# Kernel optimization log

Measured on AMD Instinct MI355X. Metric: run time of the kernel, lower is better.

## Reference

```python
import jax, jax.numpy as jnp
import numpy as np

EPS_AGG = 1e-6
EPS_BN = 1e-5
EPS_LN = 1e-5


def _bn(t, g, b):
    # BatchNorm1d in training mode: batch statistics over dim 0
    m = t.mean(0)
    v = t.var(0)
    return (t - m) * jax.lax.rsqrt(v + EPS_BN) * g + b


def _gated_gcn(x, e, src, dst, Aw, Ab, Bw, Bb, Cw, Cb, Dw, Db, Ew, Eb, gx, bx, ge, be):
    # GraphGPS GatedGCNLayer (residual=True, dropout=0, no PE)
    N = x.shape[0]
    Ax = x @ Aw + Ab
    Bx = x @ Bw + Bb
    Ce = e @ Cw + Cb
    Dx = x @ Dw + Db
    Ex = x @ Ew + Eb
    e_new = Dx[dst] + Ex[src] + Ce            # [E, D] edge gates (i=target, j=source)
    sig = jax.nn.sigmoid(e_new)
    num = jax.ops.segment_sum(sig * Bx[src], dst, num_segments=N)
    den = jax.ops.segment_sum(sig, dst, num_segments=N) + EPS_AGG
    x_new = Ax + num / den
    x = x + jax.nn.relu(_bn(x_new, gx, bx))   # BN -> ReLU -> residual
    e = e + jax.nn.relu(_bn(e_new, ge, be))
    return x, e


def setup_inputs() -> dict:
    key = jax.random.key(0)
    G, NPG, DEG, D = 256, 32, 8, 70
    NC, H = 10, 256
    N, E = G * NPG, G * NPG * DEG
    ks = list(jax.random.split(key, 24))

    def nrm(k, shape):
        return jax.random.normal(k, shape, jnp.float32)

    def lin(k, i, o):
        return nrm(k, (i, o)) / np.float32(np.sqrt(i)), jnp.zeros((o,), jnp.float32)

    x = nrm(ks[0], (N, 1))
    edge_attr = nrm(ks[1], (E, 1))
    base = jnp.repeat(jnp.arange(G, dtype=jnp.int32) * NPG, NPG * DEG)
    src = base + jax.random.randint(ks[2], (E,), 0, NPG, dtype=jnp.int32)
    dst = base + jax.random.randint(ks[3], (E,), 0, NPG, dtype=jnp.int32)
    edge_index = jnp.stack([src, dst])
    batch_index = jnp.repeat(jnp.arange(G, dtype=jnp.int32), NPG)

    inp = {"x": x, "edge_index": edge_index, "edge_attr": edge_attr, "batch_index": batch_index}
    inp["w_node"], inp["b_node"] = lin(ks[4], 1, D)
    inp["w_edge"], inp["b_edge"] = lin(ks[5], 1, D)
    i = 6
    for l in ("1", "2"):
        for nm in ("A", "B", "C", "D", "E"):
            inp[nm + l + "w"], inp[nm + l + "b"] = lin(ks[i], D, D)
            i += 1
        inp["gx" + l], inp["bx" + l] = jnp.ones((D,), jnp.float32), jnp.zeros((D,), jnp.float32)
        inp["ge" + l], inp["be" + l] = jnp.ones((D,), jnp.float32), jnp.zeros((D,), jnp.float32)
    inp["cls1_w"], inp["cls1_b"] = lin(ks[i], 2 * D, H)
    i += 1
    inp["ln_g"], inp["ln_b"] = jnp.ones((H,), jnp.float32), jnp.zeros((H,), jnp.float32)
    inp["cls2_w"], inp["cls2_b"] = lin(ks[i], H, NC)
    return inp


def reference(x, edge_index, edge_attr, batch_index,
              w_node, b_node, w_edge, b_edge,
              A1w, A1b, B1w, B1b, C1w, C1b, D1w, D1b, E1w, E1b, gx1, bx1, ge1, be1,
              A2w, A2b, B2w, B2b, C2w, C2b, D2w, D2b, E2w, E2b, gx2, bx2, ge2, be2,
              cls1_w, cls1_b, ln_g, ln_b, cls2_w, cls2_b):
    src, dst = edge_index[0], edge_index[1]
    bi = np.asarray(batch_index)
    n_iters = int(np.bincount(bi).max() // 2)   # int(max(sizes)/2)
    B = int(bi.max()) + 1

    h = x @ w_node + b_node
    e = edge_attr @ w_edge + b_edge
    h, e = _gated_gcn(h, e, src, dst, A1w, A1b, B1w, B1b, C1w, C1b, D1w, D1b, E1w, E1b, gx1, bx1, ge1, be1)
    for _ in range(n_iters):  # shared conv2 weights
        h, e = _gated_gcn(h, e, src, dst, A2w, A2b, B2w, B2b, C2w, C2b, D2w, D2b, E2w, E2b, gx2, bx2, ge2, be2)

    gmp = jax.ops.segment_max(h, batch_index, num_segments=B)
    cnt = jax.ops.segment_sum(jnp.ones((h.shape[0], 1), h.dtype), batch_index, num_segments=B)
    gap = jax.ops.segment_sum(h, batch_index, num_segments=B) / cnt
    g = jnp.concatenate([gmp, gap], axis=1)            # [B, 2*D]
    g = jax.nn.relu(g @ cls1_w + cls1_b)               # [B, 256]
    mu = g.mean(-1, keepdims=True)
    var = g.var(-1, keepdims=True)
    g = (g - mu) * jax.lax.rsqrt(var + EPS_LN) * ln_g + ln_b
    return g @ cls2_w + cls2_b                         # [B, num_classes]
```

## Files before the change

### kernel.cpp

```cpp
#include <hip/hip_runtime.h>
#include <hip/hip_fp16.h>
#include <math.h>


#define TPB 768
#define NBLK 256
#define DD 70
#define ETS 256
#define NBS 84
#define SLS 80
#define NLAYERS 17
#define SPL 280
#define NSLOT 8
#define EPS_AGG 1e-6f
#define EPS_BN 1e-5f
#define EPS_LN 1e-5f

#define SCX 0
#define SHX 72
#define SCE 144
#define SHE 216
#define SBO 288
#define BAO 360
#define BBO 432
#define ZBO 504
#define STATL_F 576

#define OFF_ET   0
#define OFF_HN   (OFF_ET + 72*ETS)
#define OFF_AX   (OFF_HN + 32*NBS)
#define OFF_BX   (OFF_AX + 32*NBS)
#define OFF_DX   (OFF_BX + 32*NBS)
#define OFF_EX   (OFF_DX + 32*NBS)
#define OFF_SLAB (OFF_EX + 32*NBS)
#define OFF_STATL (OFF_SLAB + 72*SLS)
#define SMEM_FLOATS (OFF_STATL + STATL_F)
#define SMEM_BYTES  (SMEM_FLOATS*4 + (32+33)*4 + 512 + 512 + 16)

#define EIX(k,e) (((k)<<8) + ((e) ^ ((((k)>>2)&7)<<2)))
#define SIX(j,c) (((j)<<7) + ((c) ^ ((j)&30)))

struct GPSParams {
  const float* __restrict__ x; const int* __restrict__ ei; const float* __restrict__ ea;
  const float* __restrict__ wn; const float* __restrict__ bnn;
  const float* __restrict__ we; const float* __restrict__ web;
  const float* __restrict__ Aw[2]; const float* __restrict__ Ab[2];
  const float* __restrict__ Bw[2]; const float* __restrict__ Bb[2];
  const float* __restrict__ Cw[2]; const float* __restrict__ Cb[2];
  const float* __restrict__ Dw[2]; const float* __restrict__ Db[2];
  const float* __restrict__ Ew[2]; const float* __restrict__ Eb[2];
  const float* __restrict__ gx[2]; const float* __restrict__ bx[2];
  const float* __restrict__ ge[2]; const float* __restrict__ gbe[2];
  const float* __restrict__ c1w; const float* __restrict__ c1b;
  const float* __restrict__ lng; const float* __restrict__ lnb;
  const float* __restrict__ c2w; const float* __restrict__ c2b;
  float* __restrict__ out; float* __restrict__ stats; unsigned* __restrict__ bar;
};

__device__ __forceinline__ void grid_sync(unsigned* b) {
  __syncthreads();
  if (threadIdx.x == 0) {
    unsigned g = __hip_atomic_load(b, __ATOMIC_RELAXED, __HIP_MEMORY_SCOPE_AGENT);
    int leaf = (int)(blockIdx.x >> 4);
    unsigned a = __hip_atomic_fetch_add(b + 32 + leaf*32, 1u, __ATOMIC_ACQ_REL, __HIP_MEMORY_SCOPE_AGENT);
    bool done = false;
    if (a == 15u) {
      unsigned r = __hip_atomic_fetch_add(b + 16, 1u, __ATOMIC_ACQ_REL, __HIP_MEMORY_SCOPE_AGENT);
      if (r == 15u) {
        #pragma unroll
        for (int i2 = 0; i2 < 16; ++i2)
          __hip_atomic_store(b + 32 + i2*32, 0u, __ATOMIC_RELAXED, __HIP_MEMORY_SCOPE_AGENT);
        __hip_atomic_store(b + 16, 0u, __ATOMIC_RELAXED, __HIP_MEMORY_SCOPE_AGENT);
        __hip_atomic_store(b, g + 1u, __ATOMIC_RELEASE, __HIP_MEMORY_SCOPE_AGENT);
        done = true;
      }
    }
    if (!done) {
      while (__hip_atomic_load(b, __ATOMIC_ACQUIRE, __HIP_MEMORY_SCOPE_AGENT) == g)
        __builtin_amdgcn_s_sleep(2);
    }
  }
  __syncthreads();
}

__device__ __forceinline__ void stage_wt(float* __restrict__ slab,
                                         const float* __restrict__ W, int tid) {
  for (int i = tid; i < 72*SLS; i += TPB) {
    int j = i / SLS, K = i % SLS;
    slab[i] = (j < DD && K < DD) ? W[K*DD + j] : 0.f;
  }
}

__global__ void __launch_bounds__(TPB)
__attribute__((amdgpu_waves_per_eu(3, 3)))
gps_kernel(GPSParams p) {
  extern __shared__ float smem[];
  float* eT    = smem + OFF_ET;
  float* hN    = smem + OFF_HN;
  float* Ax    = smem + OFF_AX;
  float* Bx    = smem + OFF_BX;
  float* Dx    = smem + OFF_DX;
  float* Ex    = smem + OFF_EX;
  float* slab  = smem + OFF_SLAB;
  float* statl = smem + OFF_STATL;
  unsigned* sigb = (unsigned*)(smem + OFF_DX);
  const __half* sigh = (const __half*)sigb;
  int*   icur  = (int*)(smem + SMEM_FLOATS);
  int*   ioff  = icur + 32;
  unsigned char* srcloc = (unsigned char*)(ioff + 33);
  unsigned char* dstloc = srcloc + 256;
  unsigned short* eidxS = (unsigned short*)(dstloc + 256);

  const int tid  = threadIdx.x;
  const int g    = blockIdx.x;
  const int lane = tid & 63;
  const int wid  = tid >> 6;

  const int jbe = wid * 6;
  const int e0  = lane * 4;
  const int n_kh = lane >> 5;
  const int n_n  = lane & 31;
  const int n_k0 = n_kh * 40;

  float* slot = p.stats + ((g & 7) * NLAYERS) * SPL;

  if (tid < 32) icur[tid] = 0;
  __syncthreads();
  if (tid < 256) {
    int s0 = p.ei[g*256 + tid]         - g*32;
    int d0 = p.ei[65536 + g*256 + tid] - g*32;
    srcloc[tid] = (unsigned char)s0;
    dstloc[tid] = (unsigned char)d0;
    atomicAdd(&icur[d0], 1);
  }
  __syncthreads();
  if (tid == 0) {
    int o = 0;
    for (int n = 0; n < 32; ++n) { ioff[n] = o; o += icur[n]; }
    ioff[32] = o;
  }
  __syncthreads();
  if (tid < 32) icur[tid] = ioff[tid];
  __syncthreads();
  if (tid < 256) {
    int d0 = dstloc[tid];
    int sl2 = atomicAdd(&icur[d0], 1);
    eidxS[sl2] = (unsigned short)(tid | ((int)srcloc[tid] << 8));
  }

  for (int i = tid; i < 5*32*NBS; i += TPB) hN[i] = 0.f;
  for (int i = tid; i < STATL_F; i += TPB) statl[i] = 0.f;
  for (int i = tid; i < 2*ETS; i += TPB) eT[70*ETS + i] = 0.f;
  __syncthreads();
  for (int i = tid; i < 32*DD; i += TPB) {
    int n = i / DD, j = i % DD;
    hN[n*NBS + j] = fmaf(p.x[g*32 + n], p.wn[j], p.bnn[j]);
  }
  for (int i = tid; i < DD*256; i += TPB) {
    int k = i >> 8, e = i & 255;
    eT[EIX(k, e)] = fmaf(p.ea[g*256 + e], p.we[k], p.web[k]);
  }
  __syncthreads();

  auto node_phase = [&](const float* __restrict__ W, float* __restrict__ nbuf, int boff) {
    stage_wt(slab, W, tid);
    __syncthreads();
    float acc[6];
    #pragma unroll
    for (int i = 0; i < 6; ++i) acc[i] = 0.f;
    const float* hrow = hN + n_n*NBS + n_k0;
    #pragma unroll
    for (int c = 0; c < 5; ++c) {
      float4 ha = *(const float4*)(hrow + c*8);
      float4 hb = *(const float4*)(hrow + c*8 + 4);
      #pragma unroll
      for (int i = 0; i < 6; ++i) {
        const float* wr = slab + (jbe + i)*SLS + n_k0 + c*8;
        float4 wa = *(const float4*)(wr);
        float4 wb = *(const float4*)(wr + 4);
        acc[i] = fmaf(ha.x, wa.x, acc[i]); acc[i] = fmaf(ha.y, wa.y, acc[i]);
        acc[i] = fmaf(ha.z, wa.z, acc[i]); acc[i] = fmaf(ha.w, wa.w, acc[i]);
        acc[i] = fmaf(hb.x, wb.x, acc[i]); acc[i] = fmaf(hb.y, wb.y, acc[i]);
        acc[i] = fmaf(hb.z, wb.z, acc[i]); acc[i] = fmaf(hb.w, wb.w, acc[i]);
      }
    }
    #pragma unroll
    for (int i = 0; i < 6; ++i) acc[i] += __shfl_xor(acc[i], 32, 64);
    if (n_kh == 0) {
      #pragma unroll
      for (int i = 0; i < 6; ++i) {
        int j = jbe + i;
        if (j < DD) nbuf[n_n*NBS + j] = acc[i] + statl[boff + j];
      }
    }
    __syncthreads();
  };

  #pragma unroll 1
  for (int L = 0; L < NLAYERS; ++L) {
    const int s = (L == 0) ? 0 : 1;
    float* lslot = slot + L * SPL;

    if (tid < DD) {
      statl[BAO + tid] = p.Ab[s][tid];
      statl[BBO + tid] = p.Bb[s][tid];
      statl[SBO + tid] = p.Cb[s][tid] + p.Db[s][tid] + p.Eb[s][tid];
    }
    node_phase(p.Aw[s], Ax, BAO);
    node_phase(p.Bw[s], Bx, BBO);
    node_phase(p.Dw[s], Dx, ZBO);
    node_phase(p.Ew[s], Ex, ZBO);

    stage_wt(slab, p.Cw[s], tid);
    __syncthreads();

    float acc[4][6];
    #pragma unroll
    for (int r = 0; r < 4; ++r)
      #pragma unroll
      for (int i = 0; i < 6; ++i) acc[r][i] = 0.f;

    #pragma unroll 2
    for (int c = 0; c < 18; ++c) {
      const int k0 = c*4;
      float4 ev0 = *(const float4*)(eT + EIX(k0+0, e0));
      float4 ev1 = *(const float4*)(eT + EIX(k0+1, e0));
      float4 ev2 = *(const float4*)(eT + EIX(k0+2, e0));
      float4 ev3 = *(const float4*)(eT + EIX(k0+3, e0));
      #pragma unroll
      for (int i = 0; i < 6; ++i) {
        float4 w4 = *(const float4*)(slab + (jbe + i)*SLS + k0);
        acc[0][i] = fmaf(ev0.x, w4.x, acc[0][i]); acc[1][i] = fmaf(ev0.y, w4.x, acc[1][i]);
        acc[2][i] = fmaf(ev0.z, w4.x, acc[2][i]); acc[3][i] = fmaf(ev0.w, w4.x, acc[3][i]);
        acc[0][i] = fmaf(ev1.x, w4.y, acc[0][i]); acc[1][i] = fmaf(ev1.y, w4.y, acc[1][i]);
        acc[2][i] = fmaf(ev1.z, w4.y, acc[2][i]); acc[3][i] = fmaf(ev1.w, w4.y, acc[3][i]);
        acc[0][i] = fmaf(ev2.x, w4.z, acc[0][i]); acc[1][i] = fmaf(ev2.y, w4.z, acc[1][i]);
        acc[2][i] = fmaf(ev2.z, w4.z, acc[2][i]); acc[3][i] = fmaf(ev2.w, w4.z, acc[3][i]);
        acc[0][i] = fmaf(ev3.x, w4.w, acc[0][i]); acc[1][i] = fmaf(ev3.y, w4.w, acc[1][i]);
        acc[2][i] = fmaf(ev3.z, w4.w, acc[2][i]); acc[3][i] = fmaf(ev3.w, w4.w, acc[3][i]);
      }
    }

    {
      int dl0 = dstloc[e0],   sl0 = srcloc[e0];
      int dl1 = dstloc[e0+1], sl1 = srcloc[e0+1];
      int dl2 = dstloc[e0+2], sl2 = srcloc[e0+2];
      int dl3 = dstloc[e0+3], sl3 = srcloc[e0+3];
      #pragma unroll
      for (int i = 0; i < 6; ++i) {
        int j = jbe + i;
        if (j < DD) {
          float bb = statl[SBO + j];
          acc[0][i] += Dx[dl0*NBS + j] + Ex[sl0*NBS + j] + bb;
          acc[1][i] += Dx[dl1*NBS + j] + Ex[sl1*NBS + j] + bb;
          acc[2][i] += Dx[dl2*NBS + j] + Ex[sl2*NBS + j] + bb;
          acc[3][i] += Dx[dl3*NBS + j] + Ex[sl3*NBS + j] + bb;
        }
      }
    }

    #pragma unroll
    for (int i = 0; i < 6; ++i) {
      int j = jbe + i;
      float ps = (acc[0][i] + acc[1][i]) + (acc[2][i] + acc[3][i]);
      float qs = acc[0][i]*acc[0][i];
      qs = fmaf(acc[1][i], acc[1][i], qs);
      qs = fmaf(acc[2][i], acc[2][i], qs);
      qs = fmaf(acc[3][i], acc[3][i], qs);
      #pragma unroll
      for (int d = 1; d < 64; d <<= 1) {
        ps += __shfl_xor(ps, d, 64);
        qs += __shfl_xor(qs, d, 64);
      }
      if (lane == 0 && j < DD) {
        atomicAdd(lslot + 140 + j, ps);
        atomicAdd(lslot + 210 + j, qs);
      }
    }
    __syncthreads();

    #pragma unroll
    for (int i = 0; i < 6; ++i) {
      int j = jbe + i;
      if (j < DD) {
        float s0 = 1.f / (1.f + __expf(-acc[0][i]));
        float s1 = 1.f / (1.f + __expf(-acc[1][i]));
        float s2 = 1.f / (1.f + __expf(-acc[2][i]));
        float s3 = 1.f / (1.f + __expf(-acc[3][i]));
        __half2 h01 = __floats2half2_rn(s0, s1);
        __half2 h23 = __floats2half2_rn(s2, s3);
        uint2 pk;
        pk.x = *reinterpret_cast<unsigned*>(&h01);
        pk.y = *reinterpret_cast<unsigned*>(&h23);
        *reinterpret_cast<uint2*>(sigb + SIX(j, 2*lane)) = pk;
      }
    }
    __syncthreads();

    if (tid < 576) {
      int n = tid / 18, jq = tid % 18;
      int j0 = jq * 4;
      bool v2 = (j0 + 2) < DD, v3 = (j0 + 3) < DD;
      float nm0 = 0.f, nm1 = 0.f, nm2 = 0.f, nm3 = 0.f;
      float dn0 = 0.f, dn1 = 0.f, dn2 = 0.f, dn3 = 0.f;
      int pb = ioff[n], pe = ioff[n + 1];
      for (int pp = pb; pp < pe; ++pp) {
        unsigned v = eidxS[pp];
        int e2 = v & 255, sl2 = v >> 8;
        int cb = e2 >> 1, h2 = e2 & 1;
        float s0 = __half2float(sigh[(SIX(j0+0, cb) << 1) + h2]);
        float s1 = __half2float(sigh[(SIX(j0+1, cb) << 1) + h2]);
        float s2 = v2 ? __half2float(sigh[(SIX(j0+2, cb) << 1) + h2]) : 0.f;
        float s3 = v3 ? __half2float(sigh[(SIX(j0+3, cb) << 1) + h2]) : 0.f;
        float4 b4 = *(const float4*)(Bx + sl2*NBS + j0);
        nm0 = fmaf(s0, b4.x, nm0); nm1 = fmaf(s1, b4.y, nm1);
        nm2 = fmaf(s2, b4.z, nm2); nm3 = fmaf(s3, b4.w, nm3);
        dn0 += s0; dn1 += s1; dn2 += s2; dn3 += s3;
      }
      float* axp = Ax + n*NBS + j0;
      float4 ax = *(const float4*)axp;
      ax.x += nm0 / (dn0 + EPS_AGG);
      ax.y += nm1 / (dn1 + EPS_AGG);
      ax.z += nm2 / (dn2 + EPS_AGG);
      ax.w += nm3 / (dn3 + EPS_AGG);
      *(float4*)axp = ax;
    }
    __syncthreads();

    if (tid < SPL) {
      int col = tid % DD, q = tid / DD;
      float sm = 0.f, sq = 0.f;
      #pragma unroll
      for (int r = 0; r < 8; ++r) {
        float v = Ax[(q*8 + r)*NBS + col];
        sm += v; sq = fmaf(v, v, sq);
      }
      atomicAdd(lslot + col, sm);
      atomicAdd(lslot + 70 + col, sq);
    }

    grid_sync(p.bar);

    if (tid < DD) {
      float sm = 0.f, sq = 0.f;
      #pragma unroll
      for (int sl2 = 0; sl2 < NSLOT; ++sl2) {
        const float* st = p.stats + (sl2*NLAYERS + L)*SPL;
        sm += __hip_atomic_load(st + tid,      __ATOMIC_RELAXED, __HIP_MEMORY_SCOPE_AGENT);
        sq += __hip_atomic_load(st + 70 + tid, __ATOMIC_RELAXED, __HIP_MEMORY_SCOPE_AGENT);
      }
      float mean = sm * (1.f/8192.f);
      float var  = sq * (1.f/8192.f) - mean*mean;
      float sc = p.gx[s][tid] * rsqrtf(var + EPS_BN);
      statl[SCX + tid] = sc;
      statl[SHX + tid] = fmaf(-mean, sc, p.bx[s][tid]);
    } else if (tid < 140) {
      int j = tid - DD;
      float sm = 0.f, sq = 0.f;
      #pragma unroll
      for (int sl2 = 0; sl2 < NSLOT; ++sl2) {
        const float* st = p.stats + (sl2*NLAYERS + L)*SPL;
        sm += __hip_atomic_load(st + 140 + j, __ATOMIC_RELAXED, __HIP_MEMORY_SCOPE_AGENT);
        sq += __hip_atomic_load(st + 210 + j, __ATOMIC_RELAXED, __HIP_MEMORY_SCOPE_AGENT);
      }
      float mean = sm * (1.f/65536.f);
      float var  = sq * (1.f/65536.f) - mean*mean;
      float sc = p.ge[s][j] * rsqrtf(var + EPS_BN);
      statl[SCE + j] = sc;
      statl[SHE + j] = fmaf(-mean, sc, p.gbe[s][j]);
    }
    __syncthreads();

    #pragma unroll
    for (int r = 0; r < 3; ++r) {
      int idx = tid + r*TPB;
      int n = idx / 72, j = idx - n*72;
      if (j < DD) {
        float xn = Ax[n*NBS + j];
        hN[n*NBS + j] += fmaxf(fmaf(xn, statl[SCX + j], statl[SHX + j]), 0.f);
      }
    }
    #pragma unroll
    for (int i = 0; i < 6; ++i) {
      int j = jbe + i;
      if (j < DD) {
        float sc = statl[SCE + j], sh = statl[SHE + j];
        float* ep = eT + EIX(j, e0);
        float4 eo = *(const float4*)ep;
        eo.x += fmaxf(fmaf(acc[0][i], sc, sh), 0.f);
        eo.y += fmaxf(fmaf(acc[1][i], sc, sh), 0.f);
        eo.z += fmaxf(fmaf(acc[2][i], sc, sh), 0.f);
        eo.w += fmaxf(fmaf(acc[3][i], sc, sh), 0.f);
        *(float4*)ep = eo;
      }
    }
    __syncthreads();
  }

  if (tid < DD) {
    float mx = -3.4e38f, sm = 0.f;
    #pragma unroll 4
    for (int r = 0; r < 32; ++r) {
      float v = hN[r*NBS + tid];
      mx = fmaxf(mx, v); sm += v;
    }
    statl[tid]      = mx;
    statl[70 + tid] = sm * (1.f/32.f);
  }
  __syncthreads();
  if (tid < 256) {
    float a = p.c1b[tid];
    for (int k = 0; k < DD; ++k) a = fmaf(statl[k],      p.c1w[k*256 + tid], a);
    for (int k = 0; k < DD; ++k) a = fmaf(statl[70 + k], p.c1w[(DD + k)*256 + tid], a);
    Ax[tid] = fmaxf(a, 0.f);
  }
  __syncthreads();
  if (tid == 0) {
    float sm = 0.f, sq = 0.f;
    for (int k = 0; k < 256; ++k) { float v = Ax[k]; sm += v; sq = fmaf(v, v, sq); }
    float mean = sm * (1.f/256.f);
    float var  = sq * (1.f/256.f) - mean*mean;
    statl[560] = mean;
    statl[561] = rsqrtf(var + EPS_LN);
  }
  __syncthreads();
  if (tid < 256) {
    float v = (Ax[tid] - statl[560]) * statl[561];
    Bx[tid] = fmaf(v, p.lng[tid], p.lnb[tid]);
  }
  __syncthreads();
  if (tid < 10) {
    float a = p.c2b[tid];
    for (int k = 0; k < 256; ++k) a = fmaf(Bx[k], p.c2w[k*10 + tid], a);
    p.out[g*10 + tid] = a;
  }
}

extern "C" void kernel_launch(void* const* d_in, const int* in_sizes, int n_in,
                              void* d_out, int out_size, void* d_ws, size_t ws_size,
                              hipStream_t stream) {
  (void)in_sizes; (void)n_in; (void)out_size; (void)ws_size;
  GPSParams p;
  p.x   = (const float*)d_in[0];
  p.ei  = (const int*)  d_in[1];
  p.ea  = (const float*)d_in[2];
  p.wn  = (const float*)d_in[4];  p.bnn = (const float*)d_in[5];
  p.we  = (const float*)d_in[6];  p.web = (const float*)d_in[7];
  int i = 8;
  for (int s = 0; s < 2; ++s) {
    p.Aw[s] = (const float*)d_in[i++]; p.Ab[s] = (const float*)d_in[i++];
    p.Bw[s] = (const float*)d_in[i++]; p.Bb[s] = (const float*)d_in[i++];
    p.Cw[s] = (const float*)d_in[i++]; p.Cb[s] = (const float*)d_in[i++];
    p.Dw[s] = (const float*)d_in[i++]; p.Db[s] = (const float*)d_in[i++];
    p.Ew[s] = (const float*)d_in[i++]; p.Eb[s] = (const float*)d_in[i++];
    p.gx[s] = (const float*)d_in[i++]; p.bx[s] = (const float*)d_in[i++];
    p.ge[s] = (const float*)d_in[i++]; p.gbe[s] = (const float*)d_in[i++];
  }
  p.c1w = (const float*)d_in[36]; p.c1b = (const float*)d_in[37];
  p.lng = (const float*)d_in[38]; p.lnb = (const float*)d_in[39];
  p.c2w = (const float*)d_in[40]; p.c2b = (const float*)d_in[41];
  p.out = (float*)d_out;
  p.bar = (unsigned*)d_ws;
  p.stats = (float*)((char*)d_ws + 4096);

  hipMemsetAsync(d_ws, 0, 4096 + NSLOT*NLAYERS*SPL*4, stream);

  hipFuncSetAttribute((const void*)gps_kernel,
                      hipFuncAttributeMaxDynamicSharedMemorySize, SMEM_BYTES);

  void* args[] = { (void*)&p };
  hipError_t err = hipLaunchCooperativeKernel((const void*)gps_kernel,
                                              dim3(NBLK), dim3(TPB),
                                              args, SMEM_BYTES, stream);
  if (err != hipSuccess) {
    gps_kernel<<<dim3(NBLK), dim3(TPB), SMEM_BYTES, stream>>>(p);
  }
}
```

Baseline: 1.063 ms.

## Pre-transpose weights into global workspace once and fuse four node GEMMs into one pass

Ten blocks transpose and pad all A/B/C/D/E weight matrices into a global workspace once, then a grid sync publishes them. Every block now reads weights directly from global/L2 instead of restaging each matrix into LDS five times per layer. The four separate node-projection phases, each with its own barriers, are merged into one phase where wave groups compute A, B, D and E concurrently with a 3x4 register tile. This removes many per-layer LDS staging passes and __syncthreads, at the cost of one extra grid-wide barrier and uncached-in-LDS global weight loads inside the inner loops.

Result: no change. 1.068 ms (+0.5%).

```diff
diff --git a/kernel.cpp b/kernel.cpp
--- a/kernel.cpp
+++ b/kernel.cpp
@@ -8,7 +8,7 @@
 #define DD 70
 #define ETS 256
 #define NBS 84
-#define SLS 80
+#define WTS 80
 #define NLAYERS 17
 #define SPL 280
 #define NSLOT 8
@@ -21,9 +21,6 @@
 #define SCE 144
 #define SHE 216
 #define SBO 288
-#define BAO 360
-#define BBO 432
-#define ZBO 504
 #define STATL_F 576
 
 #define OFF_ET   0
@@ -32,13 +29,16 @@
 #define OFF_BX   (OFF_AX + 32*NBS)
 #define OFF_DX   (OFF_BX + 32*NBS)
 #define OFF_EX   (OFF_DX + 32*NBS)
-#define OFF_SLAB (OFF_EX + 32*NBS)
-#define OFF_STATL (OFF_SLAB + 72*SLS)
+#define OFF_PAD  (OFF_EX + 32*NBS)
+#define OFF_STATL (OFF_PAD + 3584)
 #define SMEM_FLOATS (OFF_STATL + STATL_F)
 #define SMEM_BYTES  (SMEM_FLOATS*4 + (32+33)*4 + 512 + 512 + 16)
 
 #define EIX(k,e) (((k)<<8) + ((e) ^ ((((k)>>2)&7)<<2)))
 #define SIX(j,c) (((j)<<7) + ((c) ^ ((j)&30)))
+
+#define WS_STATS 4096
+#define WS_WT    163840
 
 struct GPSParams {
   const float* __restrict__ x; const int* __restrict__ ei; const float* __restrict__ ea;
@@ -54,7 +54,8 @@
   const float* __restrict__ c1w; const float* __restrict__ c1b;
   const float* __restrict__ lng; const float* __restrict__ lnb;
   const float* __restrict__ c2w; const float* __restrict__ c2b;
-  float* __restrict__ out; float* __restrict__ stats; unsigned* __restrict__ bar;
+  float* __restrict__ out; float* __restrict__ stats; float* __restrict__ wt;
+  unsigned* __restrict__ bar;
 };
 
 __device__ __forceinline__ void grid_sync(unsigned* b) {
@@ -83,14 +84,6 @@
   __syncthreads();
 }
 
-__device__ __forceinline__ void stage_wt(float* __restrict__ slab,
-                                         const float* __restrict__ W, int tid) {
-  for (int i = tid; i < 72*SLS; i += TPB) {
-    int j = i / SLS, K = i % SLS;
-    slab[i] = (j < DD && K < DD) ? W[K*DD + j] : 0.f;
-  }
-}
-
 __global__ void __launch_bounds__(TPB)
 __attribute__((amdgpu_waves_per_eu(3, 3)))
 gps_kernel(GPSParams p) {
@@ -101,7 +94,6 @@
   float* Bx    = smem + OFF_BX;
   float* Dx    = smem + OFF_DX;
   float* Ex    = smem + OFF_EX;
-  float* slab  = smem + OFF_SLAB;
   float* statl = smem + OFF_STATL;
   unsigned* sigb = (unsigned*)(smem + OFF_DX);
   const __half* sigh = (const __half*)sigb;
@@ -118,9 +110,9 @@
 
   const int jbe = wid * 6;
   const int e0  = lane * 4;
-  const int n_kh = lane >> 5;
-  const int n_n  = lane & 31;
-  const int n_k0 = n_kh * 40;
+  const int n_m  = wid & 3;
+  const int n_jb = (wid >> 2) * 24 + (lane >> 3) * 3;
+  const int n_n0 = (lane & 7) * 4;
 
   float* slot = p.stats + ((g & 7) * NLAYERS) * SPL;
 
@@ -148,8 +140,7 @@
     eidxS[sl2] = (unsigned short)(tid | ((int)srcloc[tid] << 8));
   }
 
-  for (int i = tid; i < 5*32*NBS; i += TPB) hN[i] = 0.f;
-  for (int i = tid; i < STATL_F; i += TPB) statl[i] = 0.f;
+  for (int i = tid; i < SMEM_FLOATS - OFF_HN; i += TPB) smem[OFF_HN + i] = 0.f;
   for (int i = tid; i < 2*ETS; i += TPB) eT[70*ETS + i] = 0.f;
   __syncthreads();
   for (int i = tid; i < 32*DD; i += TPB) {
@@ -160,65 +151,76 @@
     int k = i >> 8, e = i & 255;
     eT[EIX(k, e)] = fmaf(p.ea[g*256 + e], p.we[k], p.web[k]);
   }
-  __syncthreads();
-
-  auto node_phase = [&](const float* __restrict__ W, float* __restrict__ nbuf, int boff) {
-    stage_wt(slab, W, tid);
-    __syncthreads();
-    float acc[6];
-    #pragma unroll
-    for (int i = 0; i < 6; ++i) acc[i] = 0.f;
-    const float* hrow = hN + n_n*NBS + n_k0;
-    #pragma unroll
-    for (int c = 0; c < 5; ++c) {
-      float4 ha = *(const float4*)(hrow + c*8);
-      float4 hb = *(const float4*)(hrow + c*8 + 4);
-      #pragma unroll
-      for (int i = 0; i < 6; ++i) {
-        const float* wr = slab + (jbe + i)*SLS + n_k0 + c*8;
-        float4 wa = *(const float4*)(wr);
-        float4 wb = *(const float4*)(wr + 4);
-        acc[i] = fmaf(ha.x, wa.x, acc[i]); acc[i] = fmaf(ha.y, wa.y, acc[i]);
-        acc[i] = fmaf(ha.z, wa.z, acc[i]); acc[i] = fmaf(ha.w, wa.w, acc[i]);
-        acc[i] = fmaf(hb.x, wb.x, acc[i]); acc[i] = fmaf(hb.y, wb.y, acc[i]);
-        acc[i] = fmaf(hb.z, wb.z, acc[i]); acc[i] = fmaf(hb.w, wb.w, acc[i]);
-      }
-    }
-    #pragma unroll
-    for (int i = 0; i < 6; ++i) acc[i] += __shfl_xor(acc[i], 32, 64);
-    if (n_kh == 0) {
-      #pragma unroll
-      for (int i = 0; i < 6; ++i) {
-        int j = jbe + i;
-        if (j < DD) nbuf[n_n*NBS + j] = acc[i] + statl[boff + j];
-      }
-    }
-    __syncthreads();
-  };
+
+  if (g < 10) {
+    int ss = g / 5, mm = g % 5;
+    const float* W = (mm==0) ? p.Aw[ss] : (mm==1) ? p.Bw[ss] : (mm==2) ? p.Cw[ss]
+                   : (mm==3) ? p.Dw[ss] : p.Ew[ss];
+    float* dst = p.wt + g * (72*WTS);
+    for (int i = tid; i < 72*WTS; i += TPB) {
+      int j = i / WTS, k = i - j*WTS;
+      dst[i] = (j < DD && k < DD) ? W[k*DD + j] : 0.f;
+    }
+  }
+  grid_sync(p.bar);
 
   #pragma unroll 1
   for (int L = 0; L < NLAYERS; ++L) {
     const int s = (L == 0) ? 0 : 1;
     float* lslot = slot + L * SPL;
-
-    if (tid < DD) {
-      statl[BAO + tid] = p.Ab[s][tid];
-      statl[BBO + tid] = p.Bb[s][tid];
-      statl[SBO + tid] = p.Cb[s][tid] + p.Db[s][tid] + p.Eb[s][tid];
-    }
-    node_phase(p.Aw[s], Ax, BAO);
-    node_phase(p.Bw[s], Bx, BBO);
-    node_phase(p.Dw[s], Dx, ZBO);
-    node_phase(p.Ew[s], Ex, ZBO);
-
-    stage_wt(slab, p.Cw[s], tid);
-    __syncthreads();
-
-    float acc[4][6];
+    const float* wbase = p.wt + (size_t)(s*5) * (72*WTS);
+
+    if (tid < DD) statl[SBO + tid] = p.Cb[s][tid] + p.Db[s][tid] + p.Eb[s][tid];
+
+    {
+      const float* Wm = wbase + ((n_m==0) ? 0 : (n_m==1) ? 1 : (n_m==2) ? 3 : 4) * (72*WTS);
+      float* nbuf = (n_m==0) ? Ax : (n_m==1) ? Bx : (n_m==2) ? Dx : Ex;
+      const float* nbias = (n_m==1) ? p.Bb[s] : p.Ab[s];
+      float acc[3][4];
+      #pragma unroll
+      for (int i = 0; i < 3; ++i)
+        #pragma unroll
+        for (int n = 0; n < 4; ++n) acc[i][n] = 0.f;
+      const float* hr0 = hN + n_n0*NBS;
+      #pragma unroll 2
+      for (int c = 0; c < 18; ++c) {
+        const int k0 = c*4;
+        float4 h0 = *(const float4*)(hr0 + 0*NBS + k0);
+        float4 h1 = *(const float4*)(hr0 + 1*NBS + k0);
+        float4 h2 = *(const float4*)(hr0 + 2*NBS + k0);
+        float4 h3 = *(const float4*)(hr0 + 3*NBS + k0);
+        #pragma unroll
+        for (int i = 0; i < 3; ++i) {
+          float4 w4 = *(const float4*)(Wm + (n_jb + i)*WTS + k0);
+          acc[i][0] = fmaf(h0.x, w4.x, acc[i][0]); acc[i][0] = fmaf(h0.y, w4.y, acc[i][0]);
+          acc[i][0] = fmaf(h0.z, w4.z, acc[i][0]); acc[i][0] = fmaf(h0.w, w4.w, acc[i][0]);
+          acc[i][1] = fmaf(h1.x, w4.x, acc[i][1]); acc[i][1] = fmaf(h1.y, w4.y, acc[i][1]);
+          acc[i][1] = fmaf(h1.z, w4.z, acc[i][1]); acc[i][1] = fmaf(h1.w, w4.w, acc[i][1]);
+          acc[i][2] = fmaf(h2.x, w4.x, acc[i][2]); acc[i][2] = fmaf(h2.y, w4.y, acc[i][2]);
+          acc[i][2] = fmaf(h2.z, w4.z, acc[i][2]); acc[i][2] = fmaf(h2.w, w4.w, acc[i][2]);
+          acc[i][3] = fmaf(h3.x, w4.x, acc[i][3]); acc[i][3] = fmaf(h3.y, w4.y, acc[i][3]);
+          acc[i][3] = fmaf(h3.z, w4.z, acc[i][3]); acc[i][3] = fmaf(h3.w, w4.w, acc[i][3]);
+        }
+      }
+      #pragma unroll
+      for (int i = 0; i < 3; ++i) {
+        int j = n_jb + i;
+        if (j < DD) {
+          float b = (n_m < 2) ? nbias[j] : 0.f;
+          #pragma unroll
+          for (int n = 0; n < 4; ++n)
+            nbuf[(n_n0 + n)*NBS + j] = acc[i][n] + b;
+        }
+      }
+    }
+    __syncthreads();
+
+    const float* wC = wbase + 2 * (72*WTS);
+    float eacc[4][6];
     #pragma unroll
     for (int r = 0; r < 4; ++r)
       #pragma unroll
-      for (int i = 0; i < 6; ++i) acc[r][i] = 0.f;
+      for (int i = 0; i < 6; ++i) eacc[r][i] = 0.f;
 
     #pragma unroll 2
     for (int c = 0; c < 18; ++c) {
@@ -229,15 +231,15 @@
       float4 ev3 = *(const float4*)(eT + EIX(k0+3, e0));
       #pragma unroll
       for (int i = 0; i < 6; ++i) {
-        float4 w4 = *(const float4*)(slab + (jbe + i)*SLS + k0);
-        acc[0][i] = fmaf(ev0.x, w4.x, acc[0][i]); acc[1][i] = fmaf(ev0.y, w4.x, acc[1][i]);
-        acc[2][i] = fmaf(ev0.z, w4.x, acc[2][i]); acc[3][i] = fmaf(ev0.w, w4.x, acc[3][i]);
-        acc[0][i] = fmaf(ev1.x, w4.y, acc[0][i]); acc[1][i] = fmaf(ev1.y, w4.y, acc[1][i]);
-        acc[2][i] = fmaf(ev1.z, w4.y, acc[2][i]); acc[3][i] = fmaf(ev1.w, w4.y, acc[3][i]);
-        acc[0][i] = fmaf(ev2.x, w4.z, acc[0][i]); acc[1][i] = fmaf(ev2.y, w4.z, acc[1][i]);
-        acc[2][i] = fmaf(ev2.z, w4.z, acc[2][i]); acc[3][i] = fmaf(ev2.w, w4.z, acc[3][i]);
-        acc[0][i] = fmaf(ev3.x, w4.w, acc[0][i]); acc[1][i] = fmaf(ev3.y, w4.w, acc[1][i]);
-        acc[2][i] = fmaf(ev3.z, w4.w, acc[2][i]); acc[3][i] = fmaf(ev3.w, w4.w, acc[3][i]);
+        float4 w4 = *(const float4*)(wC + (jbe + i)*WTS + k0);
+        eacc[0][i] = fmaf(ev0.x, w4.x, eacc[0][i]); eacc[1][i] = fmaf(ev0.y, w4.x, eacc[1][i]);
+        eacc[2][i] = fmaf(ev0.z, w4.x, eacc[2][i]); eacc[3][i] = fmaf(ev0.w, w4.x, eacc[3][i]);
+        eacc[0][i] = fmaf(ev1.x, w4.y, eacc[0][i]); eacc[1][i] = fmaf(ev1.y, w4.y, eacc[1][i]);
+        eacc[2][i] = fmaf(ev1.z, w4.y, eacc[2][i]); eacc[3][i] = fmaf(ev1.w, w4.y, eacc[3][i]);
+        eacc[0][i] = fmaf(ev2.x, w4.z, eacc[0][i]); eacc[1][i] = fmaf(ev2.y, w4.z, eacc[1][i]);
+        eacc[2][i] = fmaf(ev2.z, w4.z, eacc[2][i]); eacc[3][i] = fmaf(ev2.w, w4.z, eacc[3][i]);
+        eacc[0][i] = fmaf(ev3.x, w4.w, eacc[0][i]); eacc[1][i] = fmaf(ev3.y, w4.w, eacc[1][i]);
+        eacc[2][i] = fmaf(ev3.z, w4.w, eacc[2][i]); eacc[3][i] = fmaf(ev3.w, w4.w, eacc[3][i]);
       }
     }
 
@@ -251,10 +253,10 @@
         int j = jbe + i;
         if (j < DD) {
           float bb = statl[SBO + j];
-          acc[0][i] += Dx[dl0*NBS + j] + Ex[sl0*NBS + j] + bb;
-          acc[1][i] += Dx[dl1*NBS + j] + Ex[sl1*NBS + j] + bb;
-          acc[2][i] += Dx[dl2*NBS + j] + Ex[sl2*NBS + j] + bb;
-          acc[3][i] += Dx[dl3*NBS + j] + Ex[sl3*NBS + j] + bb;
+          eacc[0][i] += Dx[dl0*NBS + j] + Ex[sl0*NBS + j] + bb;
+          eacc[1][i] += Dx[dl1*NBS + j] + Ex[sl1*NBS + j] + bb;
+          eacc[2][i] += Dx[dl2*NBS + j] + Ex[sl2*NBS + j] + bb;
+          eacc[3][i] += Dx[dl3*NBS + j] + Ex[sl3*NBS + j] + bb;
         }
       }
     }
@@ -262,11 +264,11 @@
     #pragma unroll
     for (int i = 0; i < 6; ++i) {
       int j = jbe + i;
-      float ps = (acc[0][i] + acc[1][i]) + (acc[2][i] + acc[3][i]);
-      float qs = acc[0][i]*acc[0][i];
-      qs = fmaf(acc[1][i], acc[1][i], qs);
-      qs = fmaf(acc[2][i], acc[2][i], qs);
-      qs = fmaf(acc[3][i], acc[3][i], qs);
+      float ps = (eacc[0][i] + eacc[1][i]) + (eacc[2][i] + eacc[3][i]);
+      float qs = eacc[0][i]*eacc[0][i];
+      qs = fmaf(eacc[1][i], eacc[1][i], qs);
+      qs = fmaf(eacc[2][i], eacc[2][i], qs);
+      qs = fmaf(eacc[3][i], eacc[3][i], qs);
       #pragma unroll
       for (int d = 1; d < 64; d <<= 1) {
         ps += __shfl_xor(ps, d, 64);
@@ -283,10 +285,10 @@
     for (int i = 0; i < 6; ++i) {
       int j = jbe + i;
       if (j < DD) {
-        float s0 = 1.f / (1.f + __expf(-acc[0][i]));
-        float s1 = 1.f / (1.f + __expf(-acc[1][i]));
-        float s2 = 1.f / (1.f + __expf(-acc[2][i]));
-        float s3 = 1.f / (1.f + __expf(-acc[3][i]));
+        float s0 = 1.f / (1.f + __expf(-eacc[0][i]));
+        float s1 = 1.f / (1.f + __expf(-eacc[1][i]));
+        float s2 = 1.f / (1.f + __expf(-eacc[2][i]));
+        float s3 = 1.f / (1.f + __expf(-eacc[3][i]));
         __half2 h01 = __floats2half2_rn(s0, s1);
         __half2 h23 = __floats2half2_rn(s2, s3);
         uint2 pk;
@@ -387,10 +389,10 @@
         float sc = statl[SCE + j], sh = statl[SHE + j];
         float* ep = eT + EIX(j, e0);
         float4 eo = *(const float4*)ep;
-        eo.x += fmaxf(fmaf(acc[0][i], sc, sh), 0.f);
-        eo.y += fmaxf(fmaf(acc[1][i], sc, sh), 0.f);
-        eo.z += fmaxf(fmaf(acc[2][i], sc, sh), 0.f);
-        eo.w += fmaxf(fmaf(acc[3][i], sc, sh), 0.f);
+        eo.x += fmaxf(fmaf(eacc[0][i], sc, sh), 0.f);
+        eo.y += fmaxf(fmaf(eacc[1][i], sc, sh), 0.f);
+        eo.z += fmaxf(fmaf(eacc[2][i], sc, sh), 0.f);
+        eo.w += fmaxf(fmaf(eacc[3][i], sc, sh), 0.f);
         *(float4*)ep = eo;
       }
     }
@@ -461,9 +463,10 @@
   p.c2w = (const float*)d_in[40]; p.c2b = (const float*)d_in[41];
   p.out = (float*)d_out;
   p.bar = (unsigned*)d_ws;
-  p.stats = (float*)((char*)d_ws + 4096);
-
-  hipMemsetAsync(d_ws, 0, 4096 + NSLOT*NLAYERS*SPL*4, stream);
+  p.stats = (float*)((char*)d_ws + WS_STATS);
+  p.wt    = (float*)((char*)d_ws + WS_WT);
+
+  hipMemsetAsync(d_ws, 0, WS_STATS + NSLOT*NLAYERS*SPL*4, stream);
 
   hipFuncSetAttribute((const void*)gps_kernel,
                       hipFuncAttributeMaxDynamicSharedMemorySize, SMEM_BYTES);
```
